# Performance work log

Measured on AMD Instinct MI355X. Metric: run time of the kernel, lower is better.

## Reference

```python
import jax, jax.numpy as jnp
import numpy as np

FEATURES = 8
POINTS = 3
CLASSES = 128
BATCH = 1024
TEMPERATURE = 0.1


def setup_inputs() -> dict:
    key = jax.random.key(0)
    k1, k2, k3 = jax.random.split(key, 3)
    x = jax.random.normal(k1, (BATCH, FEATURES), dtype=jnp.float32)
    beta = jax.random.uniform(k2, (FEATURES, POINTS), dtype=jnp.float32)
    classifier = jax.random.uniform(
        k3, ((POINTS + 1) ** FEATURES, CLASSES), dtype=jnp.float32)
    return {"x": x, "beta": beta, "classifier": classifier}


def reference(x, beta, classifier):
    # b: sort beta ascending per-feature, negate, cumsum, prepend a zero bin edge
    T = 1.0 / TEMPERATURE
    bneg = jnp.cumsum(-jnp.sort(beta, axis=1), axis=1)            # [F, P]
    b = jnp.concatenate(
        [jnp.zeros((beta.shape[0], 1), beta.dtype), bneg], axis=1)  # [F, P+1]
    w = jnp.arange(1, POINTS + 2, dtype=x.dtype)                  # [P+1]
    # soft one-hot binning per feature: [B, F, P+1]
    logits = (x[:, :, None] * w[None, None, :] + b[None, :, :]) * T
    hot = jax.nn.softmax(logits, axis=-1)
    # iterative outer product over features -> joint leaf histogram [B, (P+1)^F]
    B = x.shape[0]
    leaves = hot[:, 0, :]
    for f in range(1, FEATURES):  # small fixed loop over features
        leaves = (leaves[:, :, None] * hot[:, f, None, :]).reshape(B, -1)
    return leaves @ classifier  # [B, classes]
```

## Files before the change

### kernel.cpp

```cpp
#include <hip/hip_runtime.h>
#include <stdint.h>

typedef unsigned short u16;
typedef __attribute__((ext_vector_type(4))) float f32x4;
typedef __attribute__((ext_vector_type(2))) float f32x2;
typedef __attribute__((ext_vector_type(8))) short s16x8;

#define T_INV 10.0f

__device__ __forceinline__ u16 f2bf(float f) {
  uint32_t u = __float_as_uint(f);
  uint32_t r = (u + 0x7FFFu + ((u >> 16) & 1u)) >> 16;
  return (u16)r;
}

__device__ __forceinline__ void gload_lds16(const void* g, void* l) {
  __builtin_amdgcn_global_load_lds(
      (const __attribute__((address_space(1))) uint32_t*)(g),
      (__attribute__((address_space(3))) uint32_t*)(l),
      16, 0, 0);
}

__global__ __launch_bounds__(256) void k_tables(
    const float* __restrict__ x, const float* __restrict__ beta,
    u16* __restrict__ plo, float* __restrict__ phiT)
{
  const int t = threadIdx.x;
  const int b = blockIdx.x * 64 + (t >> 2);
  const int q = t & 3;

  float hot[8][4];
#pragma unroll
  for (int f = 0; f < 8; ++f) {
    float b0 = beta[f*3+0], b1 = beta[f*3+1], b2 = beta[f*3+2];
    float s0 = fminf(b0, fminf(b1, b2));
    float s2 = fmaxf(b0, fmaxf(b1, b2));
    float s1 = b0 + b1 + b2 - s0 - s2;
    float bv1 = -s0, bv2 = -(s0 + s1), bv3 = -(s0 + s1 + s2);
    float xf = x[b*8 + f];
    float l0 = (xf * 1.0f       ) * T_INV;
    float l1 = (xf * 2.0f + bv1) * T_INV;
    float l2 = (xf * 3.0f + bv2) * T_INV;
    float l3 = (xf * 4.0f + bv3) * T_INV;
    float mm = fmaxf(fmaxf(l0, l1), fmaxf(l2, l3));
    float e0 = __expf(l0 - mm), e1 = __expf(l1 - mm);
    float e2 = __expf(l2 - mm), e3 = __expf(l3 - mm);
    float inv = 1.0f / (e0 + e1 + e2 + e3);
    hot[f][0] = e0*inv; hot[f][1] = e1*inv; hot[f][2] = e2*inv; hot[f][3] = e3*inv;
  }

  {
    float h23[16];
#pragma unroll
    for (int i2 = 0; i2 < 4; ++i2)
#pragma unroll
      for (int i3 = 0; i3 < 4; ++i3) h23[i2*4+i3] = hot[2][i2] * hot[3][i3];
    float h0q = hot[0][q];
#pragma unroll
    for (int i1 = 0; i1 < 4; ++i1) {
      float c01 = h0q * hot[1][i1];
#pragma unroll
      for (int j = 0; j < 16; ++j)
        phiT[(size_t)(q*64 + i1*16 + j) * 1024 + b] = c01 * h23[j];
    }
  }
  {
    float h67[16];
#pragma unroll
    for (int i6 = 0; i6 < 4; ++i6)
#pragma unroll
      for (int i7 = 0; i7 < 4; ++i7) h67[i6*4+i7] = hot[6][i6] * hot[7][i7];
    float h4q = hot[4][q];
    u16* dst = plo + (size_t)b*256 + q*64;
#pragma unroll
    for (int i5 = 0; i5 < 4; ++i5) {
      float c45 = h4q * hot[5][i5];
#pragma unroll
      for (int j = 0; j < 16; j += 8) {
        s16x8 v;
#pragma unroll
        for (int e = 0; e < 8; ++e) v[e] = (short)f2bf(c45 * h67[j+e]);
        *(s16x8*)(dst + i5*16 + j) = v;
      }
    }
  }
}

__global__ __launch_bounds__(256) void k_transpose(
    const float* __restrict__ cls, u16* __restrict__ ct)
{
  __shared__ float tile[64 * 132];
  const int t = threadIdx.x;
  const int k0 = blockIdx.x * 64;
#pragma unroll
  for (int it = 0; it < 8; ++it) {
    int e = it * 1024 + t * 4;
    int r = e >> 7;
    int c = e & 127;
    f32x4 v = *(const f32x4*)(cls + (size_t)(k0 + r) * 128 + c);
    *(f32x4*)(tile + r * 132 + c) = v;
  }
  __syncthreads();
  const int c  = t >> 1;
  const int kh = t & 1;
  u16 vals[32];
#pragma unroll
  for (int j = 0; j < 32; ++j)
    vals[j] = f2bf(tile[(kh*32 + j) * 132 + c]);
  u16* dst = ct + (size_t)c * 65536 + k0 + kh * 32;
#pragma unroll
  for (int qq = 0; qq < 4; ++qq) {
    s16x8 v;
#pragma unroll
    for (int e2 = 0; e2 < 8; ++e2) v[e2] = (short)vals[qq*8 + e2];
    *(s16x8*)(dst + qq*8) = v;
  }
}

__global__ __launch_bounds__(512, 4) void k_main(
    const u16* __restrict__ plo, const float* __restrict__ phiT,
    const u16* __restrict__ ct, u16* __restrict__ pws)
{
  __shared__ __align__(16) u16 As[8][4096];
  __shared__ __align__(16) u16 Bb[2][4096];

  const int wg  = blockIdx.x;
  const int xcd = wg & 7;
  const int idx = wg >> 3;
  const int hig = xcd * 8 + (idx >> 3);
  const int m   = idx & 7;

  const int t    = threadIdx.x;
  const int l    = t & 63;
  const int w    = t >> 6;
  const int lrow = l & 15;
  const int kg   = l >> 4;
  const int rbase = (w & 1) * 64;
  const int cbase = (w >> 1) * 32;

  const u16* ploM = plo + (size_t)m * 128 * 256;
  const int srow = t >> 2;
  const int ssl  = t & 3;
  const int sg   = (ssl - ((srow >> 1) & 3)) & 3;

#pragma unroll
  for (int ks = 0; ks < 8; ++ks)
    gload_lds16(ploM + (size_t)srow * 256 + ks * 32 + sg * 8, &As[ks][t * 8]);

  auto stageB = [&](int h, int ks, int buf) {
    int k0 = (hig * 4 + h) * 256 + ks * 32;
    gload_lds16(ct + (size_t)srow * 65536 + k0 + sg * 8, &Bb[buf][t * 8]);
  };

  stageB(0, 0, 0);
  __syncthreads();

  f32x4 acc[4][2], hacc[4][2];
#pragma unroll
  for (int i = 0; i < 4; ++i)
#pragma unroll
    for (int j = 0; j < 2; ++j) { acc[i][j] = (f32x4)0.0f; hacc[i][j] = (f32x4)0.0f; }

#pragma unroll 1
  for (int h = 0; h < 4; ++h) {
#pragma unroll
    for (int ks = 0; ks < 8; ++ks) {
      const int buf = ks & 1;
      if (h < 3 || ks < 7) {
        int nks = (ks + 1) & 7;
        int nh  = h + (ks == 7);
        stageB(nh, nks, buf ^ 1);
      }
      s16x8 afr[4], bfr[2];
#pragma unroll
      for (int mt = 0; mt < 4; ++mt) {
        int row = rbase + mt * 16 + lrow;
        int s = (kg + ((row >> 1) & 3)) & 3;
        afr[mt] = *(const s16x8*)&As[ks][row * 32 + s * 8];
      }
#pragma unroll
      for (int nt = 0; nt < 2; ++nt) {
        int c = cbase + nt * 16 + lrow;
        int s = (kg + ((c >> 1) & 3)) & 3;
        bfr[nt] = *(const s16x8*)&Bb[buf][c * 32 + s * 8];
      }
#pragma unroll
      for (int mt = 0; mt < 4; ++mt)
#pragma unroll
        for (int nt = 0; nt < 2; ++nt)
          hacc[mt][nt] = __builtin_amdgcn_mfma_f32_16x16x32_bf16(
              afr[mt], bfr[nt], hacc[mt][nt], 0, 0, 0);
      __syncthreads();
    }
    const float* ph = phiT + (size_t)(hig * 4 + h) * 1024 + m * 128;
#pragma unroll
    for (int mt = 0; mt < 4; ++mt) {
      f32x4 p4 = *(const f32x4*)(ph + rbase + mt * 16 + kg * 4);
#pragma unroll
      for (int r = 0; r < 4; ++r) {
#pragma unroll
        for (int nt = 0; nt < 2; ++nt)
          acc[mt][nt][r] += p4[r] * hacc[mt][nt][r];
      }
#pragma unroll
      for (int nt = 0; nt < 2; ++nt) hacc[mt][nt] = (f32x4)0.0f;
    }
  }

  u16* dst = pws + ((size_t)hig * 1024 + (size_t)m * 128) * 128;
#pragma unroll
  for (int mt = 0; mt < 4; ++mt)
#pragma unroll
    for (int r = 0; r < 4; ++r) {
      int row = rbase + mt * 16 + kg * 4 + r;
#pragma unroll
      for (int nt = 0; nt < 2; ++nt) {
        int col = cbase + nt * 16 + lrow;
        dst[row * 128 + col] = f2bf(acc[mt][nt][r]);
      }
    }
}

__global__ __launch_bounds__(256) void k_reduce(
    const u16* __restrict__ p, float* __restrict__ out)
{
  const int g = blockIdx.x * 256 + threadIdx.x;
  const u16* src = p + (size_t)g * 2;
  float a0 = 0.0f, a1 = 0.0f;
#pragma unroll 8
  for (int hig = 0; hig < 64; ++hig) {
    uint32_t v = *(const uint32_t*)(src + (size_t)hig * 131072);
    a0 += __uint_as_float((v & 0xFFFFu) << 16);
    a1 += __uint_as_float(v & 0xFFFF0000u);
  }
  f32x2 o; o.x = a0; o.y = a1;
  *(f32x2*)(out + (size_t)g * 2) = o;
}

extern "C" void kernel_launch(void* const* d_in, const int* in_sizes, int n_in,
                              void* d_out, int out_size, void* d_ws, size_t ws_size,
                              hipStream_t stream)
{
  const float* x    = (const float*)d_in[0];
  const float* beta = (const float*)d_in[1];
  const float* cls  = (const float*)d_in[2];
  float* out = (float*)d_out;

  char* ws = (char*)d_ws;
  u16*   ct   = (u16*)ws;
  u16*   plo  = (u16*)(ws + (16u << 20));
  float* phiT = (float*)(ws + (16u << 20) + 524288);
  u16*   pws  = (u16*)(ws + (16u << 20) + 524288 + 1048576);

  k_tables<<<16, 256, 0, stream>>>(x, beta, plo, phiT);
  k_transpose<<<1024, 256, 0, stream>>>(cls, ct);
  k_main<<<512, 512, 0, stream>>>(plo, phiT, ct, pws);
  k_reduce<<<256, 256, 0, stream>>>(pws, out);
}
```

Before: 49.42 us.

## Load classifier B-fragments directly from global in MFMA-native layout, drop LDS staging

The transpose kernel now writes the bf16 classifier in a k-group-major layout, where each 8-element k chunk holds contiguous runs over the 128 columns, so every lane's MFMA B fragment is one 16-byte global load. The main kernel reads B fragments straight from global memory (mostly served by L2) and no longer stages them through a double-buffered LDS tile. This removes the per-k-step __syncthreads and the async LDS copies, and it precomputes the A-fragment LDS pointer once. In exchange, global-load latency is no longer hidden by explicit prefetch and has to be covered by occupancy.

```diff
diff --git a/kernel.cpp b/kernel.cpp
--- a/kernel.cpp
+++ b/kernel.cpp
@@ -107,13 +107,13 @@
 #pragma unroll
   for (int j = 0; j < 32; ++j)
     vals[j] = f2bf(tile[(kh*32 + j) * 132 + c]);
-  u16* dst = ct + (size_t)c * 65536 + k0 + kh * 32;
+  u16* dst = ct + ((size_t)(k0 >> 3) + kh * 4) * 1024 + c * 8;
 #pragma unroll
   for (int qq = 0; qq < 4; ++qq) {
     s16x8 v;
 #pragma unroll
     for (int e2 = 0; e2 < 8; ++e2) v[e2] = (short)vals[qq*8 + e2];
-    *(s16x8*)(dst + qq*8) = v;
+    *(s16x8*)(dst + (size_t)qq * 1024) = v;
   }
 }
 
@@ -122,7 +122,6 @@
     const u16* __restrict__ ct, u16* __restrict__ pws)
 {
   __shared__ __align__(16) u16 As[8][4096];
-  __shared__ __align__(16) u16 Bb[2][4096];
 
   const int wg  = blockIdx.x;
   const int xcd = wg & 7;
@@ -146,14 +145,12 @@
 #pragma unroll
   for (int ks = 0; ks < 8; ++ks)
     gload_lds16(ploM + (size_t)srow * 256 + ks * 32 + sg * 8, &As[ks][t * 8]);
-
-  auto stageB = [&](int h, int ks, int buf) {
-    int k0 = (hig * 4 + h) * 256 + ks * 32;
-    gload_lds16(ct + (size_t)srow * 65536 + k0 + sg * 8, &Bb[buf][t * 8]);
-  };
-
-  stageB(0, 0, 0);
   __syncthreads();
+
+  const int s_a = (kg + ((lrow >> 1) & 3)) & 3;
+  const u16* aP = &As[0][0] + (rbase + lrow) * 32 + s_a * 8;
+  const u16* bP = ct + (size_t)hig * 131072 + (size_t)kg * 1024
+                     + (size_t)(cbase + lrow) * 8;
 
   f32x4 acc[4][2], hacc[4][2];
 #pragma unroll
@@ -163,34 +160,22 @@
 
 #pragma unroll 1
   for (int h = 0; h < 4; ++h) {
+    const u16* bh = bP + (size_t)h * 32768;
 #pragma unroll
     for (int ks = 0; ks < 8; ++ks) {
-      const int buf = ks & 1;
-      if (h < 3 || ks < 7) {
-        int nks = (ks + 1) & 7;
-        int nh  = h + (ks == 7);
-        stageB(nh, nks, buf ^ 1);
-      }
       s16x8 afr[4], bfr[2];
 #pragma unroll
-      for (int mt = 0; mt < 4; ++mt) {
-        int row = rbase + mt * 16 + lrow;
-        int s = (kg + ((row >> 1) & 3)) & 3;
-        afr[mt] = *(const s16x8*)&As[ks][row * 32 + s * 8];
-      }
-#pragma unroll
-      for (int nt = 0; nt < 2; ++nt) {
-        int c = cbase + nt * 16 + lrow;
-        int s = (kg + ((c >> 1) & 3)) & 3;
-        bfr[nt] = *(const s16x8*)&Bb[buf][c * 32 + s * 8];
-      }
+      for (int nt = 0; nt < 2; ++nt)
+        bfr[nt] = *(const s16x8*)(bh + ks * 4096 + nt * 128);
+#pragma unroll
+      for (int mt = 0; mt < 4; ++mt)
+        afr[mt] = *(const s16x8*)(aP + ks * 4096 + mt * 512);
 #pragma unroll
       for (int mt = 0; mt < 4; ++mt)
 #pragma unroll
         for (int nt = 0; nt < 2; ++nt)
           hacc[mt][nt] = __builtin_amdgcn_mfma_f32_16x16x32_bf16(
               afr[mt], bfr[nt], hacc[mt][nt], 0, 0, 0);
-      __syncthreads();
     }
     const float* ph = phiT + (size_t)(hig * 4 + h) * 1024 + m * 128;
 #pragma unroll
```

New measurement: 105.1 us. 2.13x slower.
